# Kernel tuning notes

Hardware: AMD Instinct MI355X
Metric: run time of the kernel (lower is better)

## Reference

```python
import jax, jax.numpy as jnp
import numpy as np

B, L, D, H, NL = 2, 2048, 1024, 8, 2
HD = D // H
EPS = 1e-8


def layernorm(x, g, b):
    m = jnp.mean(x, axis=-1, keepdims=True)
    v = jnp.mean((x - m) ** 2, axis=-1, keepdims=True)
    return (x - m) / jnp.sqrt(v + EPS) * g + b


def rope(x):
    # x: [B, H, L, HD]; interleaved even/odd rotation as in the torch module
    Ls, Dh = x.shape[-2], x.shape[-1]
    pos = jnp.arange(Ls, dtype=jnp.float32)
    freqs = 1.0 / (10000.0 ** (jnp.arange(0, Dh, 2, dtype=jnp.float32) / Dh))
    ang = pos[:, None] * freqs[None, :]  # [L, HD/2]
    sin, cos = jnp.sin(ang), jnp.cos(ang)
    x1, x2 = x[..., ::2], x[..., 1::2]
    r1 = x1 * cos - x2 * sin
    r2 = x1 * sin + x2 * cos
    return jnp.stack([r1, r2], axis=-1).reshape(x.shape)


def setup_inputs() -> dict:
    key = jax.random.key(0)
    ks = jax.random.split(key, 16)
    s = 0.02

    def w(k, shape):
        return jax.random.normal(k, shape, dtype=jnp.float32) * s

    inp = {
        'seqs': jax.random.normal(ks[0], (B, L, D), dtype=jnp.float32),
        'attn_mask': jnp.broadcast_to(jnp.tril(jnp.ones((L, L), dtype=bool)), (B, L, L)),
        'Wq': w(ks[1], (NL, D, D)), 'bq': jnp.zeros((NL, D), jnp.float32),
        'Wk': w(ks[2], (NL, D, D)), 'bk': jnp.zeros((NL, D), jnp.float32),
        'Wu': w(ks[3], (NL, D, D)), 'bu': jnp.zeros((NL, D), jnp.float32),
        'Wv': w(ks[4], (NL, D, D)), 'bv': jnp.zeros((NL, D), jnp.float32),
        'Wo': w(ks[5], (NL, D, D)), 'bo': jnp.zeros((NL, D), jnp.float32),
        'W1': w(ks[6], (NL, D, D)), 'b1': jnp.zeros((NL, D), jnp.float32),
        'W2': w(ks[7], (NL, D, D)), 'b2': jnp.zeros((NL, D), jnp.float32),
        'ln1_g': jnp.ones((NL, D), jnp.float32), 'ln1_b': jnp.zeros((NL, D), jnp.float32),
        'ln2_g': jnp.ones((NL, D), jnp.float32), 'ln2_b': jnp.zeros((NL, D), jnp.float32),
        'lnf_g': jnp.ones((D,), jnp.float32), 'lnf_b': jnp.zeros((D,), jnp.float32),
    }
    return inp


def reference(seqs, attn_mask, Wq, bq, Wk, bk, Wu, bu, Wv, bv, Wo, bo,
              W1, b1, W2, b2, ln1_g, ln1_b, ln2_g, ln2_b, lnf_g, lnf_b):
    x = seqs
    Bsz, Ls, Dm = x.shape
    mask4 = attn_mask[:, None, :, :]  # [B,1,L,L]
    for i in range(NL):
        h = layernorm(x, ln1_g[i], ln1_b[i])

        def proj(Wm, bm):
            t = jnp.einsum('bld,od->blo', h, Wm) + bm
            return t.reshape(Bsz, Ls, H, HD).transpose(0, 2, 1, 3)

        Q = rope(proj(Wq[i], bq[i]))
        K = rope(proj(Wk[i], bk[i]))
        U = proj(Wu[i], bu[i])
        V = proj(Wv[i], bv[i])
        scores = jnp.einsum('bhqd,bhkd->bhqk', Q, K) / jnp.sqrt(jnp.float32(HD))
        scores = jnp.where(mask4, scores, jnp.float32(-1e9))
        wts = jax.nn.silu(scores)  # SiLU replaces softmax (HSTU)
        a = jnp.einsum('bhqk,bhkd->bhqd', wts, V) * U  # U-gated output
        a = a.transpose(0, 2, 1, 3).reshape(Bsz, Ls, Dm)
        a = jnp.einsum('bld,od->blo', a, Wo[i]) + bo[i]
        x = x + a
        h2 = layernorm(x, ln2_g[i], ln2_b[i])
        p = jnp.einsum('bld,od->blo', h2, W1[i]) + b1[i]
        f = jnp.einsum('bld,od->blo', p * jax.nn.silu(p), W2[i]) + b2[i]  # SwiGLU-style
        x = x + f
    return layernorm(x, lnf_g, lnf_b)
```

## Files before the change

kernel.cpp:

```cpp
#include <hip/hip_runtime.h>
#include <stdint.h>

typedef __attribute__((ext_vector_type(4))) float f32x4;
typedef __attribute__((ext_vector_type(8))) short s16x8;

#define D_ 1024
#define LQ 2048
#define HH_ 8
#define HD_ 128

static __device__ __forceinline__ float bf2f(ushort u){
  union { unsigned int i; float f; } v; v.i = ((unsigned int)u) << 16; return v.f;
}
static __device__ __forceinline__ ushort f2bf(float f){
  union { float f; unsigned int i; } v; v.f = f;
  unsigned int r = v.i + 0x7fffu + ((v.i >> 16) & 1u);
  return (ushort)(r >> 16);
}

struct WP { const float* s[7]; };
__global__ __launch_bounds__(256) void convert_weights(WP wp, ushort* __restrict__ dst){
  int w = blockIdx.x >> 7, blk = blockIdx.x & 127, t = threadIdx.x;
  const float4* s = (const float4*)wp.s[w];
  ushort4* d = (ushort4*)(dst + (size_t)w * 1048576);
  int base = blk * 2048 + t;
  #pragma unroll
  for (int r = 0; r < 8; r++){
    float4 v = s[base + r * 256];
    ushort4 o; o.x = f2bf(v.x); o.y = f2bf(v.y); o.z = f2bf(v.z); o.w = f2bf(v.w);
    d[base + r * 256] = o;
  }
}

template<int OUTF>
__global__ __launch_bounds__(256) void ln_kernel(const float* __restrict__ x,
    const float* __restrict__ g, const float* __restrict__ bb,
    float* __restrict__ outf, ushort* __restrict__ outb){
  int row = blockIdx.x, t = threadIdx.x;
  const float4* xr = (const float4*)(x + (size_t)row * D_);
  float4 v = xr[t];
  float s = v.x + v.y + v.z + v.w;
  float sq = v.x*v.x + v.y*v.y + v.z*v.z + v.w*v.w;
  #pragma unroll
  for (int o = 32; o; o >>= 1){ s += __shfl_down(s, o, 64); sq += __shfl_down(sq, o, 64); }
  __shared__ float red[8];
  int lane = t & 63, wv = t >> 6;
  if (!lane){ red[wv] = s; red[wv + 4] = sq; }
  __syncthreads();
  float S = red[0] + red[1] + red[2] + red[3];
  float SQ = red[4] + red[5] + red[6] + red[7];
  float m = S * (1.f / 1024.f);
  float var = SQ * (1.f / 1024.f) - m * m;
  float inv = rsqrtf(var + 1e-8f);
  float4 gv = ((const float4*)g)[t], bv = ((const float4*)bb)[t];
  float4 y;
  y.x = (v.x - m) * inv * gv.x + bv.x;
  y.y = (v.y - m) * inv * gv.y + bv.y;
  y.z = (v.z - m) * inv * gv.z + bv.z;
  y.w = (v.w - m) * inv * gv.w + bv.w;
  if (OUTF){
    ((float4*)outf)[(size_t)row * 256 + t] = y;
  } else {
    ushort4 o4; o4.x = f2bf(y.x); o4.y = f2bf(y.y); o4.z = f2bf(y.z); o4.w = f2bf(y.w);
    ((ushort4*)outb)[(size_t)row * 256 + t] = o4;
  }
}

struct P4 { ushort* d[4]; const float* b[4]; };

template<int EPI, int NB>
__global__ __launch_bounds__(256, 2) void gemm_k(
    const ushort* __restrict__ A, const ushort* __restrict__ W,
    P4 io, const float* __restrict__ resid, float* __restrict__ outf){
  __shared__ ushort As[128 * 64];
  __shared__ ushort Bs[128 * 64];
  int m0 = (blockIdx.x / NB) << 7;
  int n0 = (blockIdx.x % NB) << 7;
  int t = threadIdx.x, lane = t & 63, wv = t >> 6;
  int l15 = lane & 15, quad = lane >> 4;
  int wm = (wv & 1) << 6, wn = (wv >> 1) << 6;
  f32x4 acc[4][4] = {};
  for (int k0 = 0; k0 < 1024; k0 += 64){
    #pragma unroll
    for (int r = 0; r < 4; r++){
      int cb = r * 256 + wv * 64;
      int c = cb + lane;
      int row = c >> 3, j = c & 7;
      int kk = ((j ^ (row & 7)) << 3);
      __builtin_amdgcn_global_load_lds(
          (const __attribute__((address_space(1))) unsigned int*)(A + (size_t)(m0 + row) * 1024 + k0 + kk),
          (__attribute__((address_space(3))) unsigned int*)&As[cb * 8], 16, 0, 0);
      __builtin_amdgcn_global_load_lds(
          (const __attribute__((address_space(1))) unsigned int*)(W + (size_t)(n0 + row) * 1024 + k0 + kk),
          (__attribute__((address_space(3))) unsigned int*)&Bs[cb * 8], 16, 0, 0);
    }
    __syncthreads();
    #pragma unroll
    for (int kd = 0; kd < 2; kd++){
      s16x8 afr[4], bfr[4];
      #pragma unroll
      for (int mi = 0; mi < 4; mi++){
        int R = wm + mi * 16 + l15;
        afr[mi] = *(const s16x8*)&As[R * 64 + (((kd << 2) | quad) ^ (R & 7)) * 8];
      }
      #pragma unroll
      for (int ni = 0; ni < 4; ni++){
        int R = wn + ni * 16 + l15;
        bfr[ni] = *(const s16x8*)&Bs[R * 64 + (((kd << 2) | quad) ^ (R & 7)) * 8];
      }
      #pragma unroll
      for (int mi = 0; mi < 4; mi++)
        #pragma unroll
        for (int ni = 0; ni < 4; ni++)
          acc[mi][ni] = __builtin_amdgcn_mfma_f32_16x16x32_bf16(afr[mi], bfr[ni], acc[mi][ni], 0, 0, 0);
    }
    __syncthreads();
  }
  int sel = (EPI == 3) ? (n0 >> 10) : 0;
  ushort* dst = io.d[sel];
  const float* bias = io.b[sel];
  int ncol = (EPI == 3) ? (n0 & 1023) : n0;
  #pragma unroll
  for (int mi = 0; mi < 4; mi++){
    int gm = m0 + wm + mi * 16 + quad * 4;
    #pragma unroll
    for (int ni = 0; ni < 4; ni++){
      int cn = ncol + wn + ni * 16 + l15;
      float bv = bias[cn];
      if (EPI == 3 && sel < 2){
        int i2 = (cn & 127) >> 1;
        float freq = __builtin_amdgcn_exp2f(-0.20762050f * (float)i2);
        int odd = cn & 1;
        #pragma unroll
        for (int r = 0; r < 4; r++){
          float val = acc[mi][ni][r] + bv;
          float pv = __shfl_xor(val, 1, 64);
          int pos = (gm + r) & 2047;
          float ang = (float)pos * freq;
          float sv, cv; __sincosf(ang, &sv, &cv);
          float res = odd ? (pv * sv + val * cv) : (val * cv - pv * sv);
          dst[(size_t)(gm + r) * 1024 + cn] = f2bf(res);
        }
      } else {
        #pragma unroll
        for (int r = 0; r < 4; r++){
          float val = acc[mi][ni][r] + bv;
          size_t o = (size_t)(gm + r) * 1024 + cn;
          if (EPI == 1){ outf[o] = resid[o] + val; }
          else if (EPI == 2){
            float sg = __builtin_amdgcn_rcpf(1.f + __expf(-val));
            dst[o] = f2bf(val * val * sg);
          }
          else { dst[o] = f2bf(val); }
        }
      }
    }
  }
}

template<int EPI>
__global__ __launch_bounds__(256, 2) void gemm_k2(
    const ushort* __restrict__ A, const ushort* __restrict__ W,
    const float* __restrict__ bias, ushort* __restrict__ dst,
    const float* __restrict__ resid, float* __restrict__ outf){
  __shared__ ushort As[64 * 64];
  __shared__ ushort Bs[128 * 64];
  int m0 = (blockIdx.x >> 3) << 6;
  int n0 = (blockIdx.x & 7) << 7;
  int t = threadIdx.x, lane = t & 63, wv = t >> 6;
  int l15 = lane & 15, quad = lane >> 4;
  int wm = (wv & 1) << 5, wn = (wv >> 1) << 6;
  f32x4 acc[2][4] = {};
  for (int k0 = 0; k0 < 1024; k0 += 64){
    #pragma unroll
    for (int r = 0; r < 6; r++){
      int cb = (r < 2 ? r * 256 : (r - 2) * 256) + wv * 64;
      int c = cb + lane;
      int row = c >> 3, j = c & 7;
      int kk = ((j ^ (row & 7)) << 3);
      if (r < 2){
        __builtin_amdgcn_global_load_lds(
            (const __attribute__((address_space(1))) unsigned int*)(A + (size_t)(m0 + row) * 1024 + k0 + kk),
            (__attribute__((address_space(3))) unsigned int*)&As[cb * 8], 16, 0, 0);
      } else {
        __builtin_amdgcn_global_load_lds(
            (const __attribute__((address_space(1))) unsigned int*)(W + (size_t)(n0 + row) * 1024 + k0 + kk),
            (__attribute__((address_space(3))) unsigned int*)&Bs[cb * 8], 16, 0, 0);
      }
    }
    __syncthreads();
    #pragma unroll
    for (int kd = 0; kd < 2; kd++){
      s16x8 afr[2], bfr[4];
      #pragma unroll
      for (int mi = 0; mi < 2; mi++){
        int R = wm + mi * 16 + l15;
        afr[mi] = *(const s16x8*)&As[R * 64 + (((kd << 2) | quad) ^ (R & 7)) * 8];
      }
      #pragma unroll
      for (int ni = 0; ni < 4; ni++){
        int R = wn + ni * 16 + l15;
        bfr[ni] = *(const s16x8*)&Bs[R * 64 + (((kd << 2) | quad) ^ (R & 7)) * 8];
      }
      #pragma unroll
      for (int mi = 0; mi < 2; mi++)
        #pragma unroll
        for (int ni = 0; ni < 4; ni++)
          acc[mi][ni] = __builtin_amdgcn_mfma_f32_16x16x32_bf16(afr[mi], bfr[ni], acc[mi][ni], 0, 0, 0);
    }
    __syncthreads();
  }
  #pragma unroll
  for (int mi = 0; mi < 2; mi++){
    int gm = m0 + wm + mi * 16 + quad * 4;
    #pragma unroll
    for (int ni = 0; ni < 4; ni++){
      int cn = n0 + wn + ni * 16 + l15;
      float bv = bias[cn];
      #pragma unroll
      for (int r = 0; r < 4; r++){
        float val = acc[mi][ni][r] + bv;
        size_t o = (size_t)(gm + r) * 1024 + cn;
        if (EPI == 1){ outf[o] = resid[o] + val; }
        else {
          float sg = __builtin_amdgcn_rcpf(1.f + __expf(-val));
          dst[o] = f2bf(val * val * sg);
        }
      }
    }
  }
}

__global__ __launch_bounds__(256) void transpose_v(const ushort* __restrict__ Vb, ushort* __restrict__ Vt){
  int bidx = blockIdx.x;
  int dt = bidx & 1, lt = (bidx >> 1) & 31, bh = bidx >> 6;
  int b = bh >> 3, hh = bh & 7;
  int l0 = lt << 6, d0 = dt << 6;
  __shared__ ushort tile[64][66];
  int t = threadIdx.x;
  #pragma unroll
  for (int r = 0; r < 8; r++){
    int idx = r * 256 + t;
    int row = idx >> 5, cu = idx & 31;
    unsigned int val = *(const unsigned int*)(Vb + (size_t)(b * LQ + l0 + row) * D_ + hh * HD_ + d0 + cu * 2);
    *(unsigned int*)&tile[row][cu * 2] = val;
  }
  __syncthreads();
  #pragma unroll
  for (int r = 0; r < 8; r++){
    int idx = r * 256 + t;
    int drow = idx >> 5, lu = idx & 31;
    unsigned int val = (unsigned int)tile[lu * 2][drow] | ((unsigned int)tile[lu * 2 + 1][drow] << 16);
    *(unsigned int*)(Vt + ((size_t)(bh * HD_ + d0 + drow)) * LQ + l0 + lu * 2) = val;
  }
}

__global__ __launch_bounds__(256, 3) void attn_kernel(
    const ushort* __restrict__ Q, const ushort* __restrict__ K,
    const ushort* __restrict__ Vt,
    ushort* __restrict__ Po0, ushort* __restrict__ Po1){
  __shared__ ushort Ks[64 * 136];
  __shared__ ushort Vs[128 * 72];
  __shared__ ushort Ps[64 * 72];
  int t = threadIdx.x, lane = t & 63, wv = t >> 6;
  int l15 = lane & 15, quad = lane >> 4, q8 = quad * 8;
  int idx = blockIdx.x;
  int bh = idx & 15;
  int slot = idx >> 4;
  int qt = 31 - (slot >> 1);
  int half = slot & 1;
  int n = qt + 1;
  int c0 = (n + 1) >> 1;
  int klo = half ? c0 : 0;
  int khi = half ? n : c0;
  if (klo >= khi) return;
  int b = bh >> 3, hh = bh & 7;
  int q0 = qt << 6;
  const float scale = 0.08838834764831845f;

  s16x8 qf[4];
  const ushort* qbase = Q + (size_t)(b * LQ + q0 + (wv << 4) + l15) * D_ + hh * HD_;
  #pragma unroll
  for (int kd = 0; kd < 4; kd++) qf[kd] = *(const s16x8*)(qbase + kd * 32 + q8);

  f32x4 acc_o[8] = {};
  for (int kt = klo; kt < khi; kt++){
    int k0 = kt << 6;
    __syncthreads();
    #pragma unroll
    for (int r = 0; r < 4; r++){
      int c = r * 256 + t, row = c >> 4, ck = c & 15;
      *(s16x8*)&Ks[row * 136 + ck * 8] =
          *(const s16x8*)(K + (size_t)(b * LQ + k0 + row) * D_ + hh * HD_ + ck * 8);
    }
    #pragma unroll
    for (int r = 0; r < 4; r++){
      int c = r * 256 + t, row = c >> 3, ck = c & 7;
      *(s16x8*)&Vs[row * 72 + ck * 8] =
          *(const s16x8*)(Vt + (size_t)(bh * HD_ + row) * LQ + k0 + ck * 8);
    }
    __syncthreads();
    f32x4 sacc[4] = {};
    #pragma unroll
    for (int kd = 0; kd < 4; kd++){
      #pragma unroll
      for (int ni = 0; ni < 4; ni++){
        s16x8 bf = *(const s16x8*)&Ks[(ni * 16 + l15) * 136 + kd * 32 + q8];
        sacc[ni] = __builtin_amdgcn_mfma_f32_16x16x32_bf16(qf[kd], bf, sacc[ni], 0, 0, 0);
      }
    }
    int qg0 = q0 + (wv << 4) + quad * 4;
    #pragma unroll
    for (int ni = 0; ni < 4; ni++){
      int kg = k0 + ni * 16 + l15;
      #pragma unroll
      for (int r = 0; r < 4; r++){
        float s = sacc[ni][r] * scale;
        float p = (kg <= qg0 + r) ? (s * __builtin_amdgcn_rcpf(1.f + __expf(-s))) : 0.f;
        Ps[((wv << 4) + quad * 4 + r) * 72 + ni * 16 + l15] = f2bf(p);
      }
    }
    int prow = (wv << 4) + l15;
    #pragma unroll
    for (int kv = 0; kv < 2; kv++){
      s16x8 af = *(const s16x8*)&Ps[prow * 72 + kv * 32 + q8];
      #pragma unroll
      for (int nt = 0; nt < 8; nt++){
        s16x8 bf = *(const s16x8*)&Vs[(nt * 16 + l15) * 72 + kv * 32 + q8];
        acc_o[nt] = __builtin_amdgcn_mfma_f32_16x16x32_bf16(af, bf, acc_o[nt], 0, 0, 0);
      }
    }
  }
  ushort* Po = half ? Po1 : Po0;
  #pragma unroll
  for (int nt = 0; nt < 8; nt++){
    #pragma unroll
    for (int r = 0; r < 4; r++){
      int qg = q0 + (wv << 4) + quad * 4 + r;
      int dd = nt * 16 + l15;
      Po[(size_t)(b * LQ + qg) * D_ + hh * HD_ + dd] = f2bf(acc_o[nt][r]);
    }
  }
}

__global__ __launch_bounds__(256) void attn_reduce(
    const ushort* __restrict__ Po0, const ushort* __restrict__ Po1,
    const ushort* __restrict__ U, ushort* __restrict__ Aout){
  int i = (blockIdx.x * 256 + threadIdx.x) * 4;
  int l = (i >> 10) & 2047;
  ushort4 p0 = *(const ushort4*)(Po0 + i);
  float v0 = bf2f(p0.x), v1 = bf2f(p0.y), v2 = bf2f(p0.z), v3 = bf2f(p0.w);
  if (l >= 64){
    ushort4 p1 = *(const ushort4*)(Po1 + i);
    v0 += bf2f(p1.x); v1 += bf2f(p1.y); v2 += bf2f(p1.z); v3 += bf2f(p1.w);
  }
  ushort4 u = *(const ushort4*)(U + i);
  ushort4 o;
  o.x = f2bf(v0 * bf2f(u.x)); o.y = f2bf(v1 * bf2f(u.y));
  o.z = f2bf(v2 * bf2f(u.z)); o.w = f2bf(v3 * bf2f(u.w));
  *(ushort4*)(Aout + i) = o;
}

extern "C" void kernel_launch(void* const* d_in, const int* in_sizes, int n_in,
                              void* d_out, int out_size, void* d_ws, size_t ws_size,
                              hipStream_t stream){
  const float* seqs = (const float*)d_in[0];
  const float* bq = (const float*)d_in[3];
  const float* bk = (const float*)d_in[5];
  const float* bu = (const float*)d_in[7];
  const float* bv = (const float*)d_in[9];
  const float* bo = (const float*)d_in[11];
  const float* b1 = (const float*)d_in[13];
  const float* b2 = (const float*)d_in[15];
  const float* ln1g = (const float*)d_in[16];
  const float* ln1b = (const float*)d_in[17];
  const float* ln2g = (const float*)d_in[18];
  const float* ln2b = (const float*)d_in[19];
  const float* lnfg = (const float*)d_in[20];
  const float* lnfb = (const float*)d_in[21];

  char* base = (char*)d_ws;
  const size_t MB = 1u << 20;
  if (ws_size < 78 * MB) return;
  ushort* wbf = (ushort*)base;
  ushort* h   = (ushort*)(base + 14 * MB);
  ushort* Qb  = (ushort*)(base + 22 * MB);
  ushort* Kb  = (ushort*)(base + 30 * MB);
  ushort* Ub  = (ushort*)(base + 38 * MB);
  ushort* Vb  = (ushort*)(base + 46 * MB);
  ushort* Vt  = (ushort*)(base + 54 * MB);
  float*  xb  = (float*)(base + 62 * MB);
  ushort* ab  = h;

  const size_t DD = 1048576;
  for (int i = 0; i < 2; i++){
    WP wp;
    for (int j = 0; j < 7; j++)
      wp.s[j] = (const float*)d_in[2 + 2 * j] + (size_t)i * DD;
    convert_weights<<<7 * 128, 256, 0, stream>>>(wp, wbf);
    const ushort* Wl = wbf;
    const float* xin = (i == 0) ? seqs : xb;
    ln_kernel<0><<<4096, 256, 0, stream>>>(xin, ln1g + i * D_, ln1b + i * D_, nullptr, h);
    P4 io_qkuv = {{Qb, Kb, Ub, Vb}, {bq + i * D_, bk + i * D_, bu + i * D_, bv + i * D_}};
    gemm_k<3, 32><<<1024, 256, 0, stream>>>(h, Wl, io_qkuv, nullptr, nullptr);
    transpose_v<<<1024, 256, 0, stream>>>(Vb, Vt);
    attn_kernel<<<1024, 256, 0, stream>>>(Qb, Kb, Vt, ab, Vb);
    attn_reduce<<<4096, 256, 0, stream>>>(ab, Vb, Ub, ab);
    gemm_k2<1><<<512, 256, 0, stream>>>(ab, Wl + 4 * DD, bo + i * D_, nullptr, xin, xb);
    ln_kernel<0><<<4096, 256, 0, stream>>>(xb, ln2g + i * D_, ln2b + i * D_, nullptr, h);
    gemm_k2<2><<<512, 256, 0, stream>>>(h, Wl + 5 * DD, b1 + i * D_, Qb, nullptr, nullptr);
    gemm_k2<1><<<512, 256, 0, stream>>>(Qb, Wl + 6 * DD, b2 + i * D_, nullptr, xb, xb);
  }
  ln_kernel<1><<<4096, 256, 0, stream>>>(xb, lnfg, lnfb, (float*)d_out, nullptr);
}
```

Before: 500.4 us.

## Rewrite attention with 32x32 MFMA, register P, double-buffered async LDS loads

```diff
diff --git a/kernel.cpp b/kernel.cpp
--- a/kernel.cpp
+++ b/kernel.cpp
@@ -2,7 +2,9 @@
 #include <stdint.h>
 
 typedef __attribute__((ext_vector_type(4))) float f32x4;
+typedef __attribute__((ext_vector_type(16))) float f32x16;
 typedef __attribute__((ext_vector_type(8))) short s16x8;
+typedef __attribute__((ext_vector_type(4))) unsigned int u32x4;
 
 #define D_ 1024
 #define LQ 2048
@@ -16,6 +18,11 @@
   union { float f; unsigned int i; } v; v.f = f;
   unsigned int r = v.i + 0x7fffu + ((v.i >> 16) & 1u);
   return (ushort)(r >> 16);
+}
+static __device__ __forceinline__ unsigned int pkbf(float lo, float hi){
+  unsigned int r;
+  asm("v_cvt_pk_bf16_f32 %0, %1, %2" : "=v"(r) : "v"(lo), "v"(hi));
+  return r;
 }
 
 struct WP { const float* s[7]; };
@@ -251,94 +258,123 @@
     int idx = r * 256 + t;
     int drow = idx >> 5, lu = idx & 31;
     unsigned int val = (unsigned int)tile[lu * 2][drow] | ((unsigned int)tile[lu * 2 + 1][drow] << 16);
-    *(unsigned int*)(Vt + ((size_t)(bh * HD_ + d0 + drow)) * LQ + l0 + lu * 2) = val;
-  }
-}
-
-__global__ __launch_bounds__(256, 3) void attn_kernel(
+    int kk = lu * 2;
+    int x = kk & 15;
+    int kkp = (kk & 48) | ((x & 4) << 1) | ((x & 8) >> 1) | (x & 3);
+    *(unsigned int*)(Vt + ((size_t)(bh * HD_ + d0 + drow)) * LQ + l0 + kkp) = val;
+  }
+}
+
+__global__ __launch_bounds__(256, 2) void attn_kernel(
     const ushort* __restrict__ Q, const ushort* __restrict__ K,
     const ushort* __restrict__ Vt,
     ushort* __restrict__ Po0, ushort* __restrict__ Po1){
-  __shared__ ushort Ks[64 * 136];
-  __shared__ ushort Vs[128 * 72];
-  __shared__ ushort Ps[64 * 72];
+  __shared__ ushort Ks[2][64 * 128];
+  __shared__ ushort Vs[2][128 * 64];
   int t = threadIdx.x, lane = t & 63, wv = t >> 6;
-  int l15 = lane & 15, quad = lane >> 4, q8 = quad * 8;
+  int l31 = lane & 31, h = lane >> 5;
   int idx = blockIdx.x;
   int bh = idx & 15;
-  int slot = idx >> 4;
-  int qt = 31 - (slot >> 1);
-  int half = slot & 1;
-  int n = qt + 1;
-  int c0 = (n + 1) >> 1;
+  int s = idx >> 4;
+  int qt = (s < 16) ? (15 - (s >> 1)) : ((s - 16) >> 1);
+  int half = s & 1;
+  int ntiles = 2 * qt + 2;
+  int c0 = qt + 1;
   int klo = half ? c0 : 0;
-  int khi = half ? n : c0;
+  int khi = half ? ntiles : c0;
   if (klo >= khi) return;
   int b = bh >> 3, hh = bh & 7;
-  int q0 = qt << 6;
+  int q0 = qt << 7;
   const float scale = 0.08838834764831845f;
 
-  s16x8 qf[4];
-  const ushort* qbase = Q + (size_t)(b * LQ + q0 + (wv << 4) + l15) * D_ + hh * HD_;
-  #pragma unroll
-  for (int kd = 0; kd < 4; kd++) qf[kd] = *(const s16x8*)(qbase + kd * 32 + q8);
-
-  f32x4 acc_o[8] = {};
+  s16x8 qf[8];
+  const ushort* qbase = Q + (size_t)(b * LQ + q0 + (wv << 5) + l31) * D_ + hh * HD_;
+  #pragma unroll
+  for (int kd = 0; kd < 8; kd++) qf[kd] = *(const s16x8*)(qbase + kd * 16 + h * 8);
+
+  auto STAGE = [&](int p, int kt){
+    int k0 = kt << 6;
+    #pragma unroll
+    for (int r = 0; r < 4; r++){
+      int cb = r * 256 + (wv << 6);
+      int c = cb + lane;
+      int R = c >> 4, sl = c & 15;
+      int gg = sl ^ (R & 7);
+      __builtin_amdgcn_global_load_lds(
+          (const __attribute__((address_space(1))) unsigned int*)(K + (size_t)(b * LQ + k0 + R) * D_ + hh * HD_ + gg * 8),
+          (__attribute__((address_space(3))) unsigned int*)&Ks[p][cb * 8], 16, 0, 0);
+    }
+    #pragma unroll
+    for (int r = 0; r < 4; r++){
+      int cb = r * 256 + (wv << 6);
+      int c = cb + lane;
+      int R = c >> 3, sl = c & 7;
+      int gg = sl ^ (R & 7);
+      __builtin_amdgcn_global_load_lds(
+          (const __attribute__((address_space(1))) unsigned int*)(Vt + (size_t)(bh * HD_ + R) * LQ + k0 + gg * 8),
+          (__attribute__((address_space(3))) unsigned int*)&Vs[p][cb * 8], 16, 0, 0);
+    }
+  };
+
+  f32x16 acc_o[4] = {};
+  int qg = q0 + (wv << 5) + l31;
+
+  STAGE(0, klo);
+  __syncthreads();
   for (int kt = klo; kt < khi; kt++){
+    int p = (kt - klo) & 1;
+    if (kt + 1 < khi) STAGE(p ^ 1, kt + 1);
+    f32x16 sacc[2] = {};
+    #pragma unroll
+    for (int kd = 0; kd < 8; kd++){
+      #pragma unroll
+      for (int kb = 0; kb < 2; kb++){
+        int R = (kb << 5) + l31;
+        s16x8 af = *(const s16x8*)&Ks[p][(R * 16 + (((kd << 1) | h) ^ (R & 7))) * 8];
+        sacc[kb] = __builtin_amdgcn_mfma_f32_32x32x16_bf16(af, qf[kd], sacc[kb], 0, 0, 0);
+      }
+    }
     int k0 = kt << 6;
+    s16x8 pf[4];
+    #pragma unroll
+    for (int kb = 0; kb < 2; kb++){
+      float pvv[16];
+      #pragma unroll
+      for (int r = 0; r < 16; r++){
+        int kg = k0 + (kb << 5) + (r & 3) + ((r >> 2) << 3) + (h << 2);
+        float sv = sacc[kb][r] * scale;
+        float pp = sv * __builtin_amdgcn_rcpf(1.f + __expf(-sv));
+        pvv[r] = (kg <= qg) ? pp : 0.f;
+      }
+      #pragma unroll
+      for (int cc = 0; cc < 2; cc++){
+        union { u32x4 u; s16x8 v; } w;
+        w.u[0] = pkbf(pvv[cc*8+0], pvv[cc*8+1]);
+        w.u[1] = pkbf(pvv[cc*8+2], pvv[cc*8+3]);
+        w.u[2] = pkbf(pvv[cc*8+4], pvv[cc*8+5]);
+        w.u[3] = pkbf(pvv[cc*8+6], pvv[cc*8+7]);
+        pf[(kb << 1) | cc] = w.v;
+      }
+    }
+    #pragma unroll
+    for (int kv = 0; kv < 4; kv++){
+      #pragma unroll
+      for (int nt = 0; nt < 4; nt++){
+        int R = (nt << 5) + l31;
+        s16x8 vf = *(const s16x8*)&Vs[p][(R * 8 + (((kv << 1) | h) ^ (R & 7))) * 8];
+        acc_o[nt] = __builtin_amdgcn_mfma_f32_32x32x16_bf16(pf[kv], vf, acc_o[nt], 0, 0, 0);
+      }
+    }
     __syncthreads();
-    #pragma unroll
-    for (int r = 0; r < 4; r++){
-      int c = r * 256 + t, row = c >> 4, ck = c & 15;
-      *(s16x8*)&Ks[row * 136 + ck * 8] =
-          *(const s16x8*)(K + (size_t)(b * LQ + k0 + row) * D_ + hh * HD_ + ck * 8);
-    }
-    #pragma unroll
-    for (int r = 0; r < 4; r++){
-      int c = r * 256 + t, row = c >> 3, ck = c & 7;
-      *(s16x8*)&Vs[row * 72 + ck * 8] =
-          *(const s16x8*)(Vt + (size_t)(bh * HD_ + row) * LQ + k0 + ck * 8);
-    }
-    __syncthreads();
-    f32x4 sacc[4] = {};
-    #pragma unroll
-    for (int kd = 0; kd < 4; kd++){
-      #pragma unroll
-      for (int ni = 0; ni < 4; ni++){
-        s16x8 bf = *(const s16x8*)&Ks[(ni * 16 + l15) * 136 + kd * 32 + q8];
-        sacc[ni] = __builtin_amdgcn_mfma_f32_16x16x32_bf16(qf[kd], bf, sacc[ni], 0, 0, 0);
-      }
-    }
-    int qg0 = q0 + (wv << 4) + quad * 4;
-    #pragma unroll
-    for (int ni = 0; ni < 4; ni++){
-      int kg = k0 + ni * 16 + l15;
-      #pragma unroll
-      for (int r = 0; r < 4; r++){
-        float s = sacc[ni][r] * scale;
-        float p = (kg <= qg0 + r) ? (s * __builtin_amdgcn_rcpf(1.f + __expf(-s))) : 0.f;
-        Ps[((wv << 4) + quad * 4 + r) * 72 + ni * 16 + l15] = f2bf(p);
-      }
-    }
-    int prow = (wv << 4) + l15;
-    #pragma unroll
-    for (int kv = 0; kv < 2; kv++){
-      s16x8 af = *(const s16x8*)&Ps[prow * 72 + kv * 32 + q8];
-      #pragma unroll
-      for (int nt = 0; nt < 8; nt++){
-        s16x8 bf = *(const s16x8*)&Vs[(nt * 16 + l15) * 72 + kv * 32 + q8];
-        acc_o[nt] = __builtin_amdgcn_mfma_f32_16x16x32_bf16(af, bf, acc_o[nt], 0, 0, 0);
-      }
-    }
   }
   ushort* Po = half ? Po1 : Po0;
   #pragma unroll
-  for (int nt = 0; nt < 8; nt++){
-    #pragma unroll
-    for (int r = 0; r < 4; r++){
-      int qg = q0 + (wv << 4) + quad * 4 + r;
-      int dd = nt * 16 + l15;
-      Po[(size_t)(b * LQ + qg) * D_ + hh * HD_ + dd] = f2bf(acc_o[nt][r]);
+  for (int nt = 0; nt < 4; nt++){
+    #pragma unroll
+    for (int r = 0; r < 16; r++){
+      int qq = q0 + (wv << 5) + (r & 3) + ((r >> 2) << 3) + (h << 2);
+      int dd = (nt << 5) + l31;
+      Po[(size_t)(b * LQ + qq) * D_ + hh * HD_ + dd] = f2bf(acc_o[nt][r]);
     }
   }
 }
@@ -347,13 +383,12 @@
     const ushort* __restrict__ Po0, const ushort* __restrict__ Po1,
     const ushort* __restrict__ U, ushort* __restrict__ Aout){
   int i = (blockIdx.x * 256 + threadIdx.x) * 4;
-  int l = (i >> 10) & 2047;
   ushort4 p0 = *(const ushort4*)(Po0 + i);
-  float v0 = bf2f(p0.x), v1 = bf2f(p0.y), v2 = bf2f(p0.z), v3 = bf2f(p0.w);
-  if (l >= 64){
-    ushort4 p1 = *(const ushort4*)(Po1 + i);
-    v0 += bf2f(p1.x); v1 += bf2f(p1.y); v2 += bf2f(p1.z); v3 += bf2f(p1.w);
-  }
+  ushort4 p1 = *(const ushort4*)(Po1 + i);
+  float v0 = bf2f(p0.x) + bf2f(p1.x);
+  float v1 = bf2f(p0.y) + bf2f(p1.y);
+  float v2 = bf2f(p0.z) + bf2f(p1.z);
+  float v3 = bf2f(p0.w) + bf2f(p1.w);
   ushort4 u = *(const ushort4*)(U + i);
   ushort4 o;
   o.x = f2bf(v0 * bf2f(u.x)); o.y = f2bf(v1 * bf2f(u.y));
@@ -404,7 +439,7 @@
     P4 io_qkuv = {{Qb, Kb, Ub, Vb}, {bq + i * D_, bk + i * D_, bu + i * D_, bv + i * D_}};
     gemm_k<3, 32><<<1024, 256, 0, stream>>>(h, Wl, io_qkuv, nullptr, nullptr);
     transpose_v<<<1024, 256, 0, stream>>>(Vb, Vt);
-    attn_kernel<<<1024, 256, 0, stream>>>(Qb, Kb, Vt, ab, Vb);
+    attn_kernel<<<512, 256, 0, stream>>>(Qb, Kb, Vt, ab, Vb);
     attn_reduce<<<4096, 256, 0, stream>>>(ab, Vb, Ub, ab);
     gemm_k2<1><<<512, 256, 0, stream>>>(ab, Wl + 4 * DD, bo + i * D_, nullptr, xin, xb);
     ln_kernel<0><<<4096, 256, 0, stream>>>(xb, ln2g + i * D_, ln2b + i * D_, nullptr, h);
```

Measured after the change: 485.8 us. 1.03x faster.
